# Kernel tuning notes

Hardware: AMD Instinct MI355X
Metric: run time of the kernel (lower is better)

The kernel has to match this reference:

```python
import jax, jax.numpy as jnp
import numpy as np

B, T, N = 512, 512, 128   # batch, timesteps, driving series
M = 64                    # LSTM hidden size
UNITS = 64                # attention units


def setup_inputs() -> dict:
    key = jax.random.key(0)
    ks = jax.random.split(key, 9)
    s = lambda fan_in: 1.0 / np.sqrt(fan_in)
    return {
        "x": jax.random.normal(ks[0], (B, T, N), jnp.float32),
        "hidden_state": jax.random.normal(ks[1], (B, M), jnp.float32),
        "cell_state": jax.random.normal(ks[2], (B, M), jnp.float32),
        # Dense(units) applied to x permuted to (B, N, T): kernel contracts T
        "w1_kernel": jax.random.normal(ks[3], (T, UNITS), jnp.float32) * s(T),
        "w1_bias": jnp.zeros((UNITS,), jnp.float32),
        # Dense(units) applied to query (B, N, 2M)
        "w2_kernel": jax.random.normal(ks[4], (2 * M, UNITS), jnp.float32) * s(2 * M),
        "w2_bias": jnp.zeros((UNITS,), jnp.float32),
        # Dense(1) scoring
        "v_kernel": jax.random.normal(ks[5], (UNITS, 1), jnp.float32) * s(UNITS),
        "v_bias": jnp.zeros((1,), jnp.float32),
    }


def reference(x, hidden_state, cell_state, w1_kernel, w1_bias,
              w2_kernel, w2_bias, v_kernel, v_bias):
    # query: (B, 2M) -> broadcast over the N feature axis (RepeatVector)
    query = jnp.concatenate([hidden_state, cell_state], axis=-1)
    q_proj = query @ w2_kernel + w2_bias                    # (B, UNITS)
    x_perm = jnp.transpose(x, (0, 2, 1))                    # (B, N, T)
    score = jnp.tanh(x_perm @ w1_kernel + w1_bias + q_proj[:, None, :])  # (B, N, UNITS)
    score = score @ v_kernel + v_bias                       # (B, N, 1)
    score = jnp.transpose(score, (0, 2, 1))                 # (B, 1, N)
    attention_weights = jax.nn.softmax(score, axis=-1)      # (B, 1, N)
    context_vector = jnp.sum(attention_weights * x, axis=-1)  # (B, T)
    return context_vector, attention_weights
```

## Files before the change

kernel.cpp:

```cpp
#include <hip/hip_runtime.h>
#include <hip/hip_bf16.h>

namespace {

constexpr int kB = 512, kT = 512, kN = 128, kM = 64, kU = 64;
constexpr int XST = 520;
constexpr int RST = 18;
constexpr int CST = 528;

typedef __attribute__((ext_vector_type(8))) short short8;
typedef __attribute__((ext_vector_type(16))) float f32x16;

__device__ __forceinline__ float fb16(unsigned h) { return __uint_as_float(h << 16); }

union FragU { unsigned u[4]; uint4 q; short8 s; };

__device__ __forceinline__ unsigned bc2(__hip_bfloat162 v) {
  union { __hip_bfloat162 b; unsigned u; } c; c.b = v; return c.u;
}

__device__ __forceinline__ void pack8(const float* v, short8& hi, short8& lo) {
  FragU H, L;
#pragma unroll
  for (int jj = 0; jj < 4; ++jj) {
    float v0 = v[2 * jj], v1 = v[2 * jj + 1];
    __hip_bfloat162 h2 = __float22bfloat162_rn(float2{v0, v1});
    float h0 = __bfloat162float(h2.x), h1 = __bfloat162float(h2.y);
    __hip_bfloat162 l2 = __float22bfloat162_rn(float2{v0 - h0, v1 - h1});
    H.u[jj] = bc2(h2);
    L.u[jj] = bc2(l2);
  }
  hi = H.s; lo = L.s;
}

__device__ __forceinline__ float fast_tanh(float x) {
  return 1.0f - 2.0f / (__expf(2.0f * x) + 1.0f);
}

struct Smem {
  union {
    float red[256 * RST];
    float red2[8 * CST];
  } u;
  unsigned short xbf[kN * XST];
  float qpart[8][kU];
  float qpfull[kU];
  float sn[kN];
  float aw[kN];
};

__global__ __launch_bounds__(256) void prep_w1(const float* __restrict__ w1,
                                               unsigned* __restrict__ pwh,
                                               unsigned* __restrict__ pwl) {
  const int gid = blockIdx.x * blockDim.x + threadIdx.x;
  const int j = gid & 3, u = (gid >> 2) & 63, tg = gid >> 8;
  const int t = tg * 8 + 2 * j;
  float v0 = w1[t * kU + u], v1 = w1[(t + 1) * kU + u];
  __hip_bfloat162 h2 = __float22bfloat162_rn(float2{v0, v1});
  float h0 = __bfloat162float(h2.x), h1 = __bfloat162float(h2.y);
  __hip_bfloat162 l2 = __float22bfloat162_rn(float2{v0 - h0, v1 - h1});
  pwh[gid] = bc2(h2);
  pwl[gid] = bc2(l2);
}

__global__ __launch_bounds__(512, 2) void fused_kernel(
    const float* __restrict__ x,
    const float* __restrict__ hs,
    const float* __restrict__ cs,
    const unsigned* __restrict__ pwh,
    const unsigned* __restrict__ pwl,
    const float* __restrict__ w1b,
    const float* __restrict__ w2,
    const float* __restrict__ w2b,
    const float* __restrict__ vk,
    float* __restrict__ ctx_out,
    float* __restrict__ aw_out)
{
  extern __shared__ char smem_raw[];
  Smem& s = *reinterpret_cast<Smem*>(smem_raw);

  const int b = blockIdx.x;
  const int tid = threadIdx.x;
  const int l = tid & 63;
  const int w = tid >> 6;
  const int g = w >> 2;
  const int m = w & 3;
  const int ln = l & 31;
  const int kh = l >> 5;
  const int nA = 32 * m + ln;

  {
    const int u = tid & 63, kg = tid >> 6;
    float a0 = 0.f;
#pragma unroll
    for (int j = 0; j < 16; ++j) {
      int k = kg * 16 + j;
      float qv = (k < kM) ? hs[(size_t)b * kM + k] : cs[(size_t)b * kM + (k - kM)];
      a0 = fmaf(qv, w2[k * kU + u], a0);
    }
    s.qpart[kg][u] = a0;
  }

  f32x16 acc0, acc1;
#pragma unroll
  for (int i = 0; i < 16; ++i) { acc0[i] = 0.f; acc1[i] = 0.f; }

  const float* xb = x + (size_t)b * kT * kN;

  struct SubBuf { float rA[2][8]; uint4 rbh[2][2]; uint4 rbl[2][2]; };

  auto issue = [&](SubBuf& bf, int sub) {
    const int tb = g * 256 + sub * 32;
#pragma unroll
    for (int ks = 0; ks < 2; ++ks) {
      const int t0 = tb + ks * 16 + 8 * kh;
#pragma unroll
      for (int j = 0; j < 8; ++j)
        bf.rA[ks][j] = xb[(size_t)(t0 + j) * kN + nA];
#pragma unroll
      for (int ut = 0; ut < 2; ++ut) {
        const int base = ((t0 >> 3) * 64 + 32 * ut + ln) * 4;
        bf.rbh[ks][ut] = *(const uint4*)&pwh[base];
        bf.rbl[ks][ut] = *(const uint4*)&pwl[base];
      }
    }
  };

  auto compute = [&](SubBuf& bf, int sub) {
    const int tb = g * 256 + sub * 32;
#pragma unroll
    for (int ks = 0; ks < 2; ++ks) {
      short8 ah, al;
      pack8(bf.rA[ks], ah, al);
      const int tcur = tb + ks * 16 + 8 * kh;
      *(short8*)&s.xbf[nA * XST + tcur] = ah;
#pragma unroll
      for (int ut = 0; ut < 2; ++ut) {
        FragU BH, BL;
        BH.q = bf.rbh[ks][ut];
        BL.q = bf.rbl[ks][ut];
        f32x16& a = ut ? acc1 : acc0;
        a = __builtin_amdgcn_mfma_f32_32x32x16_bf16(ah, BH.s, a, 0, 0, 0);
        a = __builtin_amdgcn_mfma_f32_32x32x16_bf16(ah, BL.s, a, 0, 0, 0);
        a = __builtin_amdgcn_mfma_f32_32x32x16_bf16(al, BH.s, a, 0, 0, 0);
      }
    }
  };

  {
    SubBuf A_, B_;
    issue(A_, 0);
    issue(B_, 1);
#pragma unroll
    for (int s2 = 0; s2 < 8; s2 += 2) {
      compute(A_, s2);
      if (s2 + 2 < 8) issue(A_, s2 + 2);
      compute(B_, s2 + 1);
      if (s2 + 3 < 8) issue(B_, s2 + 3);
    }
  }

  __syncthreads();

  const int rrow = ((w & 3) * 64 + l) * RST;
#pragma unroll
  for (int rnd = 0; rnd < 2; ++rnd) {
    f32x16& a = rnd ? acc1 : acc0;
    if (g == 1) {
#pragma unroll
      for (int j = 0; j < 16; ++j) s.u.red[rrow + j] = a[j];
    }
    __syncthreads();
    if (g == 0) {
#pragma unroll
      for (int j = 0; j < 16; ++j) a[j] += s.u.red[rrow + j];
    }
    __syncthreads();
  }

  if (tid < kU) {
    float v = w2b[tid] + w1b[tid];
#pragma unroll
    for (int gg = 0; gg < 8; ++gg) v += s.qpart[gg][tid];
    s.qpfull[tid] = v;
  }
  __syncthreads();

  if (g == 0) {
    const float qp0 = s.qpfull[ln], qp1 = s.qpfull[32 + ln];
    const float v0 = vk[ln], v1 = vk[32 + ln];
    float pr[16];
#pragma unroll
    for (int r = 0; r < 16; ++r)
      pr[r] = fmaf(fast_tanh(acc0[r] + qp0), v0, fast_tanh(acc1[r] + qp1) * v1);
#pragma unroll
    for (int off = 1; off < 32; off <<= 1)
#pragma unroll
      for (int r = 0; r < 16; ++r)
        pr[r] += __shfl_xor(pr[r], off);
    if (ln == 0) {
#pragma unroll
      for (int r = 0; r < 16; ++r)
        s.sn[32 * m + (r & 3) + 8 * (r >> 2) + 4 * kh] = pr[r];
    }
  }
  __syncthreads();

  if (tid < 64) {
    float s0 = s.sn[tid], s1 = s.sn[tid + 64];
    float mx = fmaxf(s0, s1);
#pragma unroll
    for (int off = 32; off > 0; off >>= 1) mx = fmaxf(mx, __shfl_xor(mx, off));
    float e0 = __expf(s0 - mx), e1 = __expf(s1 - mx);
    float se = e0 + e1;
#pragma unroll
    for (int off = 32; off > 0; off >>= 1) se += __shfl_xor(se, off);
    float inv = 1.0f / se;
    float a0 = e0 * inv, a1 = e1 * inv;
    s.aw[tid] = a0;
    s.aw[tid + 64] = a1;
    aw_out[(size_t)b * kN + tid] = a0;
    aw_out[(size_t)b * kN + tid + 64] = a1;
  }
  __syncthreads();

  {
    float cp[8];
#pragma unroll
    for (int j = 0; j < 8; ++j) cp[j] = 0.f;
    const int nb = 16 * w;
#pragma unroll
    for (int nn = 0; nn < 16; ++nn) {
      const int n = nb + nn;
      const float a = s.aw[n];
      short8 xv = *(const short8*)&s.xbf[n * XST + 8 * l];
#pragma unroll
      for (int j = 0; j < 8; ++j)
        cp[j] = fmaf(fb16((unsigned)(unsigned short)xv[j]), a, cp[j]);
    }
    float4 c0 = {cp[0], cp[1], cp[2], cp[3]};
    float4 c1 = {cp[4], cp[5], cp[6], cp[7]};
    *(float4*)&s.u.red2[w * CST + 8 * l] = c0;
    *(float4*)&s.u.red2[w * CST + 8 * l + 4] = c1;
  }
  __syncthreads();
  {
    float c = 0.f;
#pragma unroll
    for (int ww = 0; ww < 8; ++ww) c += s.u.red2[ww * CST + tid];
    ctx_out[(size_t)b * kT + tid] = c;
  }
}

}

extern "C" void kernel_launch(void* const* d_in, const int* in_sizes, int n_in,
                              void* d_out, int out_size, void* d_ws, size_t ws_size,
                              hipStream_t stream) {
  const float* x   = (const float*)d_in[0];
  const float* hs  = (const float*)d_in[1];
  const float* cs  = (const float*)d_in[2];
  const float* w1  = (const float*)d_in[3];
  const float* w1b = (const float*)d_in[4];
  const float* w2  = (const float*)d_in[5];
  const float* w2b = (const float*)d_in[6];
  const float* vk  = (const float*)d_in[7];

  float* out = (float*)d_out;
  float* ctx = out;
  float* awo = out + (size_t)kB * kT;

  unsigned* pwh = (unsigned*)d_ws;
  unsigned* pwl = (unsigned*)d_ws + 16384;

  static_assert(sizeof(Smem) <= 160 * 1024, "LDS overflow");
  (void)hipFuncSetAttribute(reinterpret_cast<const void*>(fused_kernel),
                            hipFuncAttributeMaxDynamicSharedMemorySize,
                            (int)sizeof(Smem));
  hipLaunchKernelGGL(prep_w1, dim3(64), dim3(256), 0, stream, w1, pwh, pwl);
  hipLaunchKernelGGL(fused_kernel, dim3(kB), dim3(512), sizeof(Smem), stream,
                     x, hs, cs, pwh, pwl, w1b, w2, w2b, vk, ctx, awo);
}
```

Baseline: 217.9 us.

## Drop LDS x staging, shrink blocks, recompute context from global x

Each block now has 256 threads, and every wave covers the full T range. This removes the cross-group accumulator reduction through LDS and the large bf16 copy of x held in shared memory. The context vector is computed by re-reading fp32 x from global memory with a warp-shuffle dot product over N. Shared memory becomes small and launch bounds allow 4 blocks per CU, which is meant to raise occupancy and latency hiding. The cost is a second global read of x, which may or may not hit in cache, and a longer serial MFMA loop per wave.

After: 226.9 us. +4.1%, slower.

```diff
diff --git a/kernel.cpp b/kernel.cpp
--- a/kernel.cpp
+++ b/kernel.cpp
@@ -4,9 +4,6 @@
 namespace {
 
 constexpr int kB = 512, kT = 512, kN = 128, kM = 64, kU = 64;
-constexpr int XST = 520;
-constexpr int RST = 18;
-constexpr int CST = 528;
 
 typedef __attribute__((ext_vector_type(8))) short short8;
 typedef __attribute__((ext_vector_type(16))) float f32x16;
@@ -38,12 +35,7 @@
 }
 
 struct Smem {
-  union {
-    float red[256 * RST];
-    float red2[8 * CST];
-  } u;
-  unsigned short xbf[kN * XST];
-  float qpart[8][kU];
+  float qpart[4][kU];
   float qpfull[kU];
   float sn[kN];
   float aw[kN];
@@ -63,7 +55,7 @@
   pwl[gid] = bc2(l2);
 }
 
-__global__ __launch_bounds__(512, 2) void fused_kernel(
+__global__ __launch_bounds__(256, 4) void fused_kernel(
     const float* __restrict__ x,
     const float* __restrict__ hs,
     const float* __restrict__ cs,
@@ -76,25 +68,22 @@
     float* __restrict__ ctx_out,
     float* __restrict__ aw_out)
 {
-  extern __shared__ char smem_raw[];
-  Smem& s = *reinterpret_cast<Smem*>(smem_raw);
+  __shared__ Smem s;
 
   const int b = blockIdx.x;
   const int tid = threadIdx.x;
   const int l = tid & 63;
   const int w = tid >> 6;
-  const int g = w >> 2;
-  const int m = w & 3;
   const int ln = l & 31;
   const int kh = l >> 5;
-  const int nA = 32 * m + ln;
+  const int nA = 32 * w + ln;
 
   {
     const int u = tid & 63, kg = tid >> 6;
     float a0 = 0.f;
 #pragma unroll
-    for (int j = 0; j < 16; ++j) {
-      int k = kg * 16 + j;
+    for (int j = 0; j < 32; ++j) {
+      int k = kg * 32 + j;
       float qv = (k < kM) ? hs[(size_t)b * kM + k] : cs[(size_t)b * kM + (k - kM)];
       a0 = fmaf(qv, w2[k * kU + u], a0);
     }
@@ -110,7 +99,7 @@
   struct SubBuf { float rA[2][8]; uint4 rbh[2][2]; uint4 rbl[2][2]; };
 
   auto issue = [&](SubBuf& bf, int sub) {
-    const int tb = g * 256 + sub * 32;
+    const int tb = sub * 32;
 #pragma unroll
     for (int ks = 0; ks < 2; ++ks) {
       const int t0 = tb + ks * 16 + 8 * kh;
@@ -126,14 +115,11 @@
     }
   };
 
-  auto compute = [&](SubBuf& bf, int sub) {
-    const int tb = g * 256 + sub * 32;
+  auto compute = [&](SubBuf& bf) {
 #pragma unroll
     for (int ks = 0; ks < 2; ++ks) {
       short8 ah, al;
       pack8(bf.rA[ks], ah, al);
-      const int tcur = tb + ks * 16 + 8 * kh;
-      *(short8*)&s.xbf[nA * XST + tcur] = ah;
 #pragma unroll
       for (int ut = 0; ut < 2; ++ut) {
         FragU BH, BL;
@@ -152,41 +138,25 @@
     issue(A_, 0);
     issue(B_, 1);
 #pragma unroll
-    for (int s2 = 0; s2 < 8; s2 += 2) {
-      compute(A_, s2);
-      if (s2 + 2 < 8) issue(A_, s2 + 2);
-      compute(B_, s2 + 1);
-      if (s2 + 3 < 8) issue(B_, s2 + 3);
-    }
-  }
-
-  __syncthreads();
-
-  const int rrow = ((w & 3) * 64 + l) * RST;
-#pragma unroll
-  for (int rnd = 0; rnd < 2; ++rnd) {
-    f32x16& a = rnd ? acc1 : acc0;
-    if (g == 1) {
-#pragma unroll
-      for (int j = 0; j < 16; ++j) s.u.red[rrow + j] = a[j];
-    }
-    __syncthreads();
-    if (g == 0) {
-#pragma unroll
-      for (int j = 0; j < 16; ++j) a[j] += s.u.red[rrow + j];
-    }
-    __syncthreads();
-  }
+    for (int s2 = 0; s2 < 16; s2 += 2) {
+      compute(A_);
+      if (s2 + 2 < 16) issue(A_, s2 + 2);
+      compute(B_);
+      if (s2 + 3 < 16) issue(B_, s2 + 3);
+    }
+  }
+
+  __syncthreads();
 
   if (tid < kU) {
     float v = w2b[tid] + w1b[tid];
 #pragma unroll
-    for (int gg = 0; gg < 8; ++gg) v += s.qpart[gg][tid];
+    for (int gg = 0; gg < 4; ++gg) v += s.qpart[gg][tid];
     s.qpfull[tid] = v;
   }
   __syncthreads();
 
-  if (g == 0) {
+  {
     const float qp0 = s.qpfull[ln], qp1 = s.qpfull[32 + ln];
     const float v0 = vk[ln], v1 = vk[32 + ln];
     float pr[16];
@@ -201,7 +171,7 @@
     if (ln == 0) {
 #pragma unroll
       for (int r = 0; r < 16; ++r)
-        s.sn[32 * m + (r & 3) + 8 * (r >> 2) + 4 * kh] = pr[r];
+        s.sn[32 * w + (r & 3) + 8 * (r >> 2) + 4 * kh] = pr[r];
     }
   }
   __syncthreads();
@@ -225,30 +195,29 @@
   __syncthreads();
 
   {
-    float cp[8];
-#pragma unroll
-    for (int j = 0; j < 8; ++j) cp[j] = 0.f;
-    const int nb = 16 * w;
-#pragma unroll
-    for (int nn = 0; nn < 16; ++nn) {
-      const int n = nb + nn;
-      const float a = s.aw[n];
-      short8 xv = *(const short8*)&s.xbf[n * XST + 8 * l];
-#pragma unroll
-      for (int j = 0; j < 8; ++j)
-        cp[j] = fmaf(fb16((unsigned)(unsigned short)xv[j]), a, cp[j]);
-    }
-    float4 c0 = {cp[0], cp[1], cp[2], cp[3]};
-    float4 c1 = {cp[4], cp[5], cp[6], cp[7]};
-    *(float4*)&s.u.red2[w * CST + 8 * l] = c0;
-    *(float4*)&s.u.red2[w * CST + 8 * l + 4] = c1;
-  }
-  __syncthreads();
-  {
-    float c = 0.f;
-#pragma unroll
-    for (int ww = 0; ww < 8; ++ww) c += s.u.red2[ww * CST + tid];
-    ctx_out[(size_t)b * kT + tid] = c;
+    const float4 av = *(const float4*)&s.aw[4 * ln];
+    const int tbase = 128 * w;
+    float o0 = 0.f, o1 = 0.f;
+#pragma unroll 8
+    for (int r = 0; r < 32; ++r) {
+      const int t = tbase + 2 * r + kh;
+      float4 v = *(const float4*)&xb[(size_t)t * kN + 4 * ln];
+      float p = fmaf(v.x, av.x, fmaf(v.y, av.y, fmaf(v.z, av.z, v.w * av.w)));
+#pragma unroll
+      for (int off = 1; off < 32; off <<= 1) p += __shfl_xor(p, off);
+      if (ln == r) o0 = p;
+    }
+#pragma unroll 8
+    for (int r = 0; r < 32; ++r) {
+      const int t = tbase + 64 + 2 * r + kh;
+      float4 v = *(const float4*)&xb[(size_t)t * kN + 4 * ln];
+      float p = fmaf(v.x, av.x, fmaf(v.y, av.y, fmaf(v.z, av.z, v.w * av.w)));
+#pragma unroll
+      for (int off = 1; off < 32; off <<= 1) p += __shfl_xor(p, off);
+      if (ln == r) o1 = p;
+    }
+    ctx_out[(size_t)b * kT + tbase + 2 * ln + kh] = o0;
+    ctx_out[(size_t)b * kT + tbase + 64 + 2 * ln + kh] = o1;
   }
 }
 
@@ -273,11 +242,7 @@
   unsigned* pwh = (unsigned*)d_ws;
   unsigned* pwl = (unsigned*)d_ws + 16384;
 
-  static_assert(sizeof(Smem) <= 160 * 1024, "LDS overflow");
-  (void)hipFuncSetAttribute(reinterpret_cast<const void*>(fused_kernel),
-                            hipFuncAttributeMaxDynamicSharedMemorySize,
-                            (int)sizeof(Smem));
   hipLaunchKernelGGL(prep_w1, dim3(64), dim3(256), 0, stream, w1, pwh, pwl);
-  hipLaunchKernelGGL(fused_kernel, dim3(kB), dim3(512), sizeof(Smem), stream,
+  hipLaunchKernelGGL(fused_kernel, dim3(kB), dim3(256), 0, stream,
                      x, hs, cs, pwh, pwl, w1b, w2, w2b, vk, ctx, awo);
 }
```
